# Optimization experiments

Measured on AMD Instinct MI355X. Metric: run time of the kernel, lower is better.

The kernel has to match this reference:

```python
import jax, jax.numpy as jnp
import numpy as np

D_MODEL = 1024
NUM_HEADS = 16
HEAD_DIM = D_MODEL // NUM_HEADS
THETA = 10000.0


def _init_linear(key, d_out, d_in):
    sigma = np.sqrt(2.0 / (d_in + d_out))
    w = jax.random.truncated_normal(key, -3.0, 3.0, (d_out, d_in), dtype=jnp.float32)
    return w * sigma


def setup_inputs() -> dict:
    key = jax.random.key(0)
    kh, kq, kk, kv, ko = jax.random.split(key, 5)
    h = jax.random.normal(kh, (2, 2048, D_MODEL), dtype=jnp.float32)
    return {
        "h": h,
        "wq": _init_linear(kq, D_MODEL, D_MODEL),
        "wk": _init_linear(kk, D_MODEL, D_MODEL),
        "wv": _init_linear(kv, D_MODEL, D_MODEL),
        "wo": _init_linear(ko, D_MODEL, D_MODEL),
    }


def _rope(x, pos):
    # x: [B, H, T, dh]; rotate interleaved pairs (..., 2k, 2k+1)
    dh = x.shape[-1]
    freq = THETA ** (-jnp.arange(0, dh // 2, dtype=jnp.float32) / (dh // 2))
    ang = pos[:, None] * freq[None, :]            # [T, dh/2]
    cos, sin = jnp.cos(ang), jnp.sin(ang)
    xr = x.reshape(*x.shape[:-1], dh // 2, 2)
    x0, x1 = xr[..., 0], xr[..., 1]
    out = jnp.stack((cos * x0 - sin * x1, sin * x0 + cos * x1), axis=-1)
    return out.reshape(x.shape)


def reference(h, wq, wk, wv, wo):
    B, T, D = h.shape
    Hn, dh = NUM_HEADS, HEAD_DIM

    def split_heads(x):  # [B,T,D] -> [B,H,T,dh]
        return x.reshape(B, T, Hn, dh).transpose(0, 2, 1, 3)

    Q = split_heads(h @ wq.T)
    K = split_heads(h @ wk.T)
    V = split_heads(h @ wv.T)

    pos = jnp.arange(T, dtype=jnp.float32)
    Q = _rope(Q, pos)
    K = _rope(K, pos)

    scores = jnp.einsum('bhqd,bhkd->bhqk', Q, K) / jnp.sqrt(jnp.float32(dh))
    mask = jnp.tril(jnp.ones((T, T), dtype=bool))
    scores = jnp.where(mask, scores, -jnp.inf)
    attn = jax.nn.softmax(scores, axis=-1)
    out = jnp.einsum('bhqk,bhkd->bhqd', attn, V)   # [B,H,T,dh]
    out = out.transpose(0, 2, 1, 3).reshape(B, T, D)
    return out @ wo.T
```

## Files before the change

kernel.cpp:

```cpp
#include <hip/hip_runtime.h>
#include <math.h>

typedef __bf16 bf16_t;
typedef __bf16 v8bf __attribute__((ext_vector_type(8)));
typedef __bf16 v4bf __attribute__((ext_vector_type(4)));
typedef float  v4f  __attribute__((ext_vector_type(4)));

#define AS1 __attribute__((address_space(1)))
#define AS3 __attribute__((address_space(3)))

static __device__ __forceinline__ void load_lds16(const bf16_t* g, bf16_t* l) {
    __builtin_amdgcn_global_load_lds((AS1 void*)const_cast<bf16_t*>(g),
                                     (AS3 void*)l, 16, 0, 0);
}
static __device__ __forceinline__ void load_lds16b(const char* g, char* l) {
    __builtin_amdgcn_global_load_lds((AS1 void*)const_cast<char*>(g),
                                     (AS3 void*)l, 16, 0, 0);
}

static __device__ __forceinline__ void fast_sincos(float ang, float* sn, float* cs) {
    float rv = ang * 0.15915494309189535f;
    rv -= floorf(rv);
    const float a = rv * 6.283185307179586f;
    *sn = __sinf(a);
    *cs = __cosf(a);
}

__global__ __launch_bounds__(256) void cvt_fp32_bf16(
    const float* __restrict__ h,  const float* __restrict__ wq,
    const float* __restrict__ wk, const float* __restrict__ wv,
    const float* __restrict__ wo,
    bf16_t* __restrict__ hb,  bf16_t* __restrict__ wqb,
    bf16_t* __restrict__ wkb, bf16_t* __restrict__ wvb,
    bf16_t* __restrict__ wob)
{
    const size_t HM = (size_t)4 << 20;
    const size_t i8 = ((size_t)blockIdx.x * 256 + threadIdx.x) * 8;
    const float* src; bf16_t* dst; size_t off;
    if (i8 < HM) { src = h; dst = hb; off = i8; }
    else {
        const size_t r = (i8 - HM) >> 20;
        off = (i8 - HM) & (((size_t)1 << 20) - 1);
        src = (r == 0) ? wq  : (r == 1) ? wk  : (r == 2) ? wv  : wo;
        dst = (r == 0) ? wqb : (r == 1) ? wkb : (r == 2) ? wvb : wob;
    }
    const float4 a = *(const float4*)(src + off);
    const float4 b = *(const float4*)(src + off + 4);
    v8bf o;
    o[0]=(bf16_t)a.x; o[1]=(bf16_t)a.y; o[2]=(bf16_t)a.z; o[3]=(bf16_t)a.w;
    o[4]=(bf16_t)b.x; o[5]=(bf16_t)b.y; o[6]=(bf16_t)b.z; o[7]=(bf16_t)b.w;
    *(v8bf*)(dst + off) = o;
}

__global__ __launch_bounds__(256) void qkv_gemm_rope(
    const bf16_t* __restrict__ A,
    const bf16_t* __restrict__ wq,
    const bf16_t* __restrict__ wk,
    const bf16_t* __restrict__ wv,
    bf16_t* __restrict__ qo, bf16_t* __restrict__ ko, bf16_t* __restrict__ vo)
{
    __shared__ __align__(16) bf16_t smem[17408];

    const int tid = threadIdx.x;
    const int n0  = blockIdx.x * 128;
    const int m0  = blockIdx.y * 128;
    const int sel = n0 >> 10;
    const bf16_t* W = (sel == 0) ? wq : (sel == 1) ? wk : wv;
    const int wr0 = n0 & 1023;

    const int wave = tid >> 6;
    const int lane = tid & 63;
    const int l16  = lane & 15;
    const int quad = lane >> 4;
    const int wrow = (wave >> 1) * 64;
    const int wcol = (wave & 1) * 64;

    v4f acc[4][4];
    #pragma unroll
    for (int i = 0; i < 4; ++i)
        #pragma unroll
        for (int j = 0; j < 4; ++j) acc[i][j] = (v4f)(0.0f);

    const int c0r  = tid >> 2;
    const int c0c  = (tid & 3) * 8;
    #define QKV_STAGE(bbuf, ktile)                                             \
        {                                                                      \
            const int k0_ = (ktile) * 32;                                      \
            load_lds16(A + (size_t)(m0 + c0r) * 1024 + k0_ + c0c,              \
                       smem + (bbuf) * 4096 + tid * 8);                        \
            load_lds16(A + (size_t)(m0 + 64 + c0r) * 1024 + k0_ + c0c,         \
                       smem + (bbuf) * 4096 + 2048 + tid * 8);                 \
            load_lds16(W + (size_t)(wr0 + c0r) * 1024 + k0_ + c0c,             \
                       smem + 8192 + (bbuf) * 4096 + tid * 8);                 \
            load_lds16(W + (size_t)(wr0 + 64 + c0r) * 1024 + k0_ + c0c,        \
                       smem + 8192 + (bbuf) * 4096 + 2048 + tid * 8);          \
        }

    QKV_STAGE(0, 0);
    for (int kt = 0; kt < 32; ++kt) {
        const int cur = kt & 1;
        __syncthreads();
        if (kt < 31) QKV_STAGE(cur ^ 1, kt + 1);

        const bf16_t* As = smem + cur * 4096;
        const bf16_t* Bs = smem + 8192 + cur * 4096;
        v8bf af[4], bfb[4];
        #pragma unroll
        for (int i = 0; i < 4; ++i) {
            af[i]  = *(const v8bf*)&As[(wrow + i * 16 + l16) * 32 + quad * 8];
            bfb[i] = *(const v8bf*)&Bs[(wcol + i * 16 + l16) * 32 + quad * 8];
        }
        #pragma unroll
        for (int i = 0; i < 4; ++i)
            #pragma unroll
            for (int j = 0; j < 4; ++j)
                acc[i][j] = __builtin_amdgcn_mfma_f32_16x16x32_bf16(
                    af[i], bfb[j], acc[i][j], 0, 0, 0);
    }
    __syncthreads();
    #undef QKV_STAGE

    bf16_t* Ls = smem + wave * 4352;
    const int bq     = (m0 + wrow) >> 11;
    const int hd     = ((n0 + wcol) >> 6) & 15;
    const int t_base = (m0 + wrow) & 2047;

    if (sel < 2) {
        bf16_t* OUT = (sel == 0) ? qo : ko;
        #pragma unroll
        for (int j = 0; j < 4; ++j) {
            const int dcol = j * 16 + l16;
            const int kk   = dcol >> 1;
            const float f  = exp2f((float)kk * -0.4152410118609203f);
            float cb, sb, c1, s1, c16, s16;
            fast_sincos((float)(t_base + quad * 4) * f, &sb, &cb);
            fast_sincos(f, &s1, &c1);
            fast_sincos(16.0f * f, &s16, &c16);
            float ci = cb, si = sb;
            #pragma unroll
            for (int i = 0; i < 4; ++i) {
                float cr = ci, sr = si;
                #pragma unroll
                for (int r = 0; r < 4; ++r) {
                    const int mrow = i * 16 + quad * 4 + r;
                    float v = acc[i][j][r];
                    const float vp = __shfl_xor(v, 1);
                    v = ((dcol & 1) == 0) ? (cr * v - sr * vp)
                                          : (sr * vp + cr * v);
                    Ls[mrow * 68 + dcol] = (bf16_t)v;
                    if (r < 3) {
                        const float cn = cr * c1 - sr * s1;
                        sr = sr * c1 + cr * s1;
                        cr = cn;
                    }
                }
                if (i < 3) {
                    const float cn = ci * c16 - si * s16;
                    si = si * c16 + ci * s16;
                    ci = cn;
                }
            }
        }
        #pragma unroll
        for (int s = 0; s < 8; ++s) {
            const int row = s * 8 + (lane >> 3);
            const int off = (lane & 7) * 8;
            const v8bf vv = *(const v8bf*)&Ls[row * 68 + off];
            *(v8bf*)(OUT + (((size_t)(bq * 16 + hd) * 2048) + t_base + row) * 64 + off) = vv;
        }
    } else {
        #pragma unroll
        for (int i = 0; i < 4; ++i)
            #pragma unroll
            for (int j = 0; j < 4; ++j) {
                v4bf p;
                #pragma unroll
                for (int r = 0; r < 4; ++r) p[r] = (bf16_t)acc[i][j][r];
                *(v4bf*)&Ls[(j * 16 + l16) * 68 + i * 16 + quad * 4] = p;
            }
        #pragma unroll
        for (int s = 0; s < 8; ++s) {
            const int drow = s * 8 + (lane >> 3);
            const int off  = (lane & 7) * 8;
            const v8bf vv = *(const v8bf*)&Ls[drow * 68 + off];
            *(v8bf*)(vo + (((size_t)(bq * 16 + hd) * 64) + drow) * 2048 + t_base + off) = vv;
        }
    }
}

__global__ __launch_bounds__(256, 4) void attn_mfma(
    const bf16_t* __restrict__ qg,
    const bf16_t* __restrict__ kg,
    const bf16_t* __restrict__ vtg,
    bf16_t* __restrict__ og)
{
    __shared__ __align__(16) bf16_t Ks[2][4096];
    __shared__ __align__(16) bf16_t Vs[2][4096];
    __shared__ __align__(16) bf16_t Ps[4][1024];

    const int tid  = threadIdx.x;
    const int wave = tid >> 6;
    const int lane = tid & 63;
    const int l16  = lane & 15;
    const int quad = lane >> 4;

    const int i   = blockIdx.x;
    const int xcd = i & 7;
    const int j   = i >> 3;
    const int bhl = j >> 5;
    const int u   = j & 31;
    const int q64 = (bhl & 1) ? (31 - u) : u;
    const int bh  = xcd * 4 + bhl;
    const int b = bh >> 4, hh = bh & 15;

    const char* Kb = (const char*)(kg  + (size_t)bh * 2048 * 64);
    const char* Vb = (const char*)(vtg + (size_t)bh * 64 * 2048);

    const int qglb = q64 * 64 + wave * 16 + l16;

    const int sw  = (l16 & 7) << 4;
    const int cb0 = (quad << 4) ^ sw;

    const int grow = tid >> 3;
    const int gsw  = ((tid & 7) << 4) ^ ((grow & 7) << 4);

    const bf16_t* qrow = qg + ((size_t)bh * 2048 + qglb) * 64;
    v8bf qf[2];
    qf[0] = *(const v8bf*)(qrow + quad * 8);
    qf[1] = *(const v8bf*)(qrow + 32 + quad * 8);
    #pragma unroll
    for (int e = 0; e < 8; ++e) {
        qf[0][e] = (bf16_t)((float)qf[0][e] * 0.18033688011112042f);
        qf[1][e] = (bf16_t)((float)qf[1][e] * 0.18033688011112042f);
    }

    v8bf ones1;
    #pragma unroll
    for (int e = 0; e < 8; ++e) ones1[e] = (bf16_t)1.0f;

    float m_r = -1e30f;
    v4f l_acc = (v4f)(0.0f);
    v4f o_acc[4];
    #pragma unroll
    for (int d = 0; d < 4; ++d) o_acc[d] = (v4f)(0.0f);

    {
        const char* ks = Kb + ((size_t)grow << 7) + gsw;
        const char* vs = Vb + ((size_t)grow << 12) + gsw;
        char* kd = (char*)Ks[0] + tid * 16;
        char* vd = (char*)Vs[0] + tid * 16;
        load_lds16b(ks, kd);
        load_lds16b(ks + (32 << 7), kd + 4096);
        load_lds16b(vs, vd);
        load_lds16b(vs + ((size_t)32 << 12), vd + 4096);
    }

    for (int kt = 0; kt <= q64; ++kt) {
        const int cur = kt & 1;
        const int nxt = cur ^ 1;
        __syncthreads();

        if (kt < q64) {
            const char* ks = Kb + ((size_t)((kt + 1) * 64 + grow) << 7) + gsw;
            const char* vs = Vb + ((size_t)grow << 12) + ((size_t)(kt + 1) << 7) + gsw;
            char* kd = (char*)Ks[nxt] + tid * 16;
            char* vd = (char*)Vs[nxt] + tid * 16;
            load_lds16b(ks, kd);
            load_lds16b(ks + (32 << 7), kd + 4096);
            load_lds16b(vs, vd);
            load_lds16b(vs + ((size_t)32 << 12), vd + 4096);
        }

        const char* ksc = (const char*)Ks[cur];
        v4f s_acc[4];
        #pragma unroll
        for (int kblk = 0; kblk < 4; ++kblk) s_acc[kblk] = (v4f)(0.0f);
        #pragma unroll
        for (int kblk = 0; kblk < 4; ++kblk) {
            const char* kr = ksc + ((kblk * 16 + l16) << 7);
            const v8bf kf0 = *(const v8bf*)(kr + cb0);
            const v8bf kf1 = *(const v8bf*)(kr + (cb0 ^ 64));
            s_acc[kblk] = __builtin_amdgcn_mfma_f32_16x16x32_bf16(
                kf0, qf[0], s_acc[kblk], 0, 0, 0);
            s_acc[kblk] = __builtin_amdgcn_mfma_f32_16x16x32_bf16(
                kf1, qf[1], s_acc[kblk], 0, 0, 0);
        }

        if (kt == q64) {
            #pragma unroll
            for (int kblk = 0; kblk < 4; ++kblk)
                #pragma unroll
                for (int r = 0; r < 4; ++r)
                    if (kt * 64 + kblk * 16 + quad * 4 + r > qglb)
                        s_acc[kblk][r] = -1e30f;
        }

        float mx = -1e30f;
        #pragma unroll
        for (int kblk = 0; kblk < 4; ++kblk)
            #pragma unroll
            for (int r = 0; r < 4; ++r) mx = fmaxf(mx, s_acc[kblk][r]);
        mx = fmaxf(mx, __shfl_xor(mx, 16));
        mx = fmaxf(mx, __shfl_xor(mx, 32));
        if (!__all(mx - m_r <= 8.0f)) {
            const float mn = fmaxf(m_r, mx);
            const float a  = exp2f(m_r - mn);
            m_r = mn;
            l_acc *= a;
            #pragma unroll
            for (int d = 0; d < 4; ++d) o_acc[d] *= a;
        }

        char* psc = (char*)Ps[wave] + (l16 << 7);
        #pragma unroll
        for (int kblk = 0; kblk < 4; ++kblk) {
            v4bf p;
            #pragma unroll
            for (int r = 0; r < 4; ++r)
                p[r] = (bf16_t)exp2f(s_acc[kblk][r] - m_r);
            *(v4bf*)(psc + ((kblk * 32 + quad * 8) ^ sw)) = p;
        }
        const v8bf pf0 = *(const v8bf*)(psc + cb0);
        const v8bf pf1 = *(const v8bf*)(psc + (cb0 ^ 64));

        const char* vsc = (const char*)Vs[cur];
        #pragma unroll
        for (int dblk = 0; dblk < 4; ++dblk) {
            const char* vr = vsc + ((dblk * 16 + l16) << 7);
            const v8bf vf0 = *(const v8bf*)(vr + cb0);
            const v8bf vf1 = *(const v8bf*)(vr + (cb0 ^ 64));
            o_acc[dblk] = __builtin_amdgcn_mfma_f32_16x16x32_bf16(
                vf0, pf0, o_acc[dblk], 0, 0, 0);
            o_acc[dblk] = __builtin_amdgcn_mfma_f32_16x16x32_bf16(
                vf1, pf1, o_acc[dblk], 0, 0, 0);
        }
        l_acc = __builtin_amdgcn_mfma_f32_16x16x32_bf16(ones1, pf0, l_acc, 0, 0, 0);
        l_acc = __builtin_amdgcn_mfma_f32_16x16x32_bf16(ones1, pf1, l_acc, 0, 0, 0);
    }

    const float inv_l = 1.0f / l_acc[0];
    const size_t base = ((size_t)b * 2048 + qglb) * 1024 + hh * 64;
    #pragma unroll
    for (int dblk = 0; dblk < 4; ++dblk) {
        v4bf o;
        #pragma unroll
        for (int r = 0; r < 4; ++r) o[r] = (bf16_t)(o_acc[dblk][r] * inv_l);
        *(v4bf*)(og + base + dblk * 16 + quad * 4) = o;
    }
}

__global__ __launch_bounds__(256) void out_gemm(
    const bf16_t* __restrict__ A,
    const bf16_t* __restrict__ W,
    float* __restrict__ C)
{
    __shared__ __align__(16) float smemf[6144];
    bf16_t* Sb = (bf16_t*)smemf;

    const int tid = threadIdx.x;
    const int n0  = blockIdx.x * 64;
    const int m0  = blockIdx.y * 128;

    const int wave = tid >> 6;
    const int lane = tid & 63;
    const int l16  = lane & 15;
    const int quad = lane >> 4;
    const int wrow = (wave >> 1) * 64;
    const int wcol = (wave & 1) * 32;

    v4f acc[4][2];
    #pragma unroll
    for (int i = 0; i < 4; ++i)
        #pragma unroll
        for (int j = 0; j < 2; ++j) acc[i][j] = (v4f)(0.0f);

    const int c0r = tid >> 2;
    const int c0c = (tid & 3) * 8;
    #define OUT_STAGE(bbuf, ktile)                                             \
        {                                                                      \
            const int k0_ = (ktile) * 32;                                      \
            load_lds16(A + (size_t)(m0 + c0r) * 1024 + k0_ + c0c,              \
                       Sb + (bbuf) * 4096 + tid * 8);                          \
            load_lds16(A + (size_t)(m0 + 64 + c0r) * 1024 + k0_ + c0c,         \
                       Sb + (bbuf) * 4096 + 2048 + tid * 8);                   \
            load_lds16(W + (size_t)(n0 + (tid >> 2)) * 1024 + k0_ + c0c,       \
                       Sb + 8192 + (bbuf) * 2048 + tid * 8);                   \
        }

    OUT_STAGE(0, 0);
    for (int kt = 0; kt < 32; ++kt) {
        const int cur = kt & 1;
        __syncthreads();
        if (kt < 31) OUT_STAGE(cur ^ 1, kt + 1);

        const bf16_t* As = Sb + cur * 4096;
        const bf16_t* Bs = Sb + 8192 + cur * 2048;
        v8bf af[4], bfb[2];
        #pragma unroll
        for (int i = 0; i < 4; ++i)
            af[i]  = *(const v8bf*)&As[(wrow + i * 16 + l16) * 32 + quad * 8];
        #pragma unroll
        for (int j = 0; j < 2; ++j)
            bfb[j] = *(const v8bf*)&Bs[(wcol + j * 16 + l16) * 32 + quad * 8];
        #pragma unroll
        for (int i = 0; i < 4; ++i)
            #pragma unroll
            for (int j = 0; j < 2; ++j)
                acc[i][j] = __builtin_amdgcn_mfma_f32_16x16x32_bf16(
                    af[i], bfb[j], acc[i][j], 0, 0, 0);
    }
    __syncthreads();
    #undef OUT_STAGE

    float* Lw = smemf + wave * 1088;
    #pragma unroll
    for (int half = 0; half < 2; ++half) {
        #pragma unroll
        for (int ii = 0; ii < 2; ++ii) {
            const int i = half * 2 + ii;
            #pragma unroll
            for (int j = 0; j < 2; ++j)
                #pragma unroll
                for (int r = 0; r < 4; ++r)
                    Lw[(ii * 16 + quad * 4 + r) * 34 + j * 16 + l16] = acc[i][j][r];
        }
        #pragma unroll
        for (int s = 0; s < 8; ++s) {
            const int row = s * 4 + (lane >> 4);
            const float2 vv = *(const float2*)&Lw[row * 34 + l16 * 2];
            *(float2*)(C + (size_t)(m0 + wrow + half * 32 + row) * 1024
                         + n0 + wcol + l16 * 2) = vv;
        }
    }
}

extern "C" void kernel_launch(void* const* d_in, const int* in_sizes, int n_in,
                              void* d_out, int out_size, void* d_ws, size_t ws_size,
                              hipStream_t stream) {
    const float* h  = (const float*)d_in[0];
    const float* wq = (const float*)d_in[1];
    const float* wk = (const float*)d_in[2];
    const float* wv = (const float*)d_in[3];
    const float* wo = (const float*)d_in[4];

    const size_t NH = (size_t)4096 * 1024;
    const size_t NW = (size_t)1024 * 1024;

    bf16_t* hb  = (bf16_t*)d_ws;
    bf16_t* wqb = hb  + NH;
    bf16_t* wkb = wqb + NW;
    bf16_t* wvb = wkb + NW;
    bf16_t* wob = wvb + NW;
    bf16_t* qw  = wob + NW;
    bf16_t* kw  = qw + NH;
    bf16_t* vw  = kw + NH;
    bf16_t* og  = hb;

    cvt_fp32_bf16<<<dim3(4096), dim3(256), 0, stream>>>(
        h, wq, wk, wv, wo, hb, wqb, wkb, wvb, wob);
    qkv_gemm_rope<<<dim3(24, 32), dim3(256), 0, stream>>>(
        hb, wqb, wkb, wvb, qw, kw, vw);
    attn_mfma<<<dim3(1024), dim3(256), 0, stream>>>(qw, kw, vw, og);
    out_gemm<<<dim3(16, 32), dim3(256), 0, stream>>>(og, wob, (float*)d_out);
}
```

Measured before the change: 186.6 us.

## Use single-buffered 128-key tiles in causal attention kernel

The attention kernel now processes 128 keys per iteration instead of 64. It drops the double-buffered K/V prefetch in favour of a single load-then-sync per tile, and launch bounds move from 4 to 3 waves per SIMD. This halves loop iterations and barriers and gives each wave more MFMA work per sync. In exchange, global-to-LDS loads no longer overlap compute, and for odd query tiles the last key tile computes a masked half that is thrown away.

```diff
diff --git a/kernel.cpp b/kernel.cpp
--- a/kernel.cpp
+++ b/kernel.cpp
@@ -188,15 +188,15 @@
     }
 }
 
-__global__ __launch_bounds__(256, 4) void attn_mfma(
+__global__ __launch_bounds__(256, 3) void attn_mfma(
     const bf16_t* __restrict__ qg,
     const bf16_t* __restrict__ kg,
     const bf16_t* __restrict__ vtg,
     bf16_t* __restrict__ og)
 {
-    __shared__ __align__(16) bf16_t Ks[2][4096];
-    __shared__ __align__(16) bf16_t Vs[2][4096];
-    __shared__ __align__(16) bf16_t Ps[4][1024];
+    __shared__ __align__(16) bf16_t Ks[8192];
+    __shared__ __align__(16) bf16_t Vs[8192];
+    __shared__ __align__(16) bf16_t Ps[4][2048];
 
     const int tid  = threadIdx.x;
     const int wave = tid >> 6;
@@ -209,20 +209,23 @@
     const int j   = i >> 3;
     const int bhl = j >> 5;
     const int u   = j & 31;
-    const int q64 = (bhl & 1) ? (31 - u) : u;
+    const int qt  = (bhl & 1) ? (31 - u) : u;
     const int bh  = xcd * 4 + bhl;
     const int b = bh >> 4, hh = bh & 15;
 
     const char* Kb = (const char*)(kg  + (size_t)bh * 2048 * 64);
     const char* Vb = (const char*)(vtg + (size_t)bh * 64 * 2048);
 
-    const int qglb = q64 * 64 + wave * 16 + l16;
+    const int qglb = qt * 64 + wave * 16 + l16;
+    const int ktb  = qt >> 1;
 
     const int sw  = (l16 & 7) << 4;
     const int cb0 = (quad << 4) ^ sw;
 
-    const int grow = tid >> 3;
-    const int gsw  = ((tid & 7) << 4) ^ ((grow & 7) << 4);
+    const int krow = tid >> 3;
+    const int kswb = ((tid & 7) << 4) ^ ((krow & 7) << 4);
+    const int vrow = tid >> 4;
+    const int vswb = ((tid & 15) << 4) ^ ((vrow & 7) << 4);
 
     const bf16_t* qrow = qg + ((size_t)bh * 2048 + qglb) * 64;
     v8bf qf[2];
@@ -244,40 +247,28 @@
     #pragma unroll
     for (int d = 0; d < 4; ++d) o_acc[d] = (v4f)(0.0f);
 
-    {
-        const char* ks = Kb + ((size_t)grow << 7) + gsw;
-        const char* vs = Vb + ((size_t)grow << 12) + gsw;
-        char* kd = (char*)Ks[0] + tid * 16;
-        char* vd = (char*)Vs[0] + tid * 16;
-        load_lds16b(ks, kd);
-        load_lds16b(ks + (32 << 7), kd + 4096);
-        load_lds16b(vs, vd);
-        load_lds16b(vs + ((size_t)32 << 12), vd + 4096);
-    }
-
-    for (int kt = 0; kt <= q64; ++kt) {
-        const int cur = kt & 1;
-        const int nxt = cur ^ 1;
+    for (int kt = 0; kt <= ktb; ++kt) {
+        if (kt) __syncthreads();
+
+        {
+            const char* ksrc = Kb + ((size_t)(kt * 128 + krow) << 7) + kswb;
+            const char* vsrc = Vb + ((size_t)vrow << 12) + ((size_t)kt << 8) + vswb;
+            char* kd = (char*)Ks + tid * 16;
+            char* vd = (char*)Vs + tid * 16;
+            #pragma unroll
+            for (int s = 0; s < 4; ++s) {
+                load_lds16b(ksrc + (size_t)s * (32 << 7), kd + s * 4096);
+                load_lds16b(vsrc + ((size_t)s << 16), vd + s * 4096);
+            }
+        }
         __syncthreads();
 
-        if (kt < q64) {
-            const char* ks = Kb + ((size_t)((kt + 1) * 64 + grow) << 7) + gsw;
-            const char* vs = Vb + ((size_t)grow << 12) + ((size_t)(kt + 1) << 7) + gsw;
-            char* kd = (char*)Ks[nxt] + tid * 16;
-            char* vd = (char*)Vs[nxt] + tid * 16;
-            load_lds16b(ks, kd);
-            load_lds16b(ks + (32 << 7), kd + 4096);
-            load_lds16b(vs, vd);
-            load_lds16b(vs + ((size_t)32 << 12), vd + 4096);
-        }
-
-        const char* ksc = (const char*)Ks[cur];
-        v4f s_acc[4];
-        #pragma unroll
-        for (int kblk = 0; kblk < 4; ++kblk) s_acc[kblk] = (v4f)(0.0f);
-        #pragma unroll
-        for (int kblk = 0; kblk < 4; ++kblk) {
-            const char* kr = ksc + ((kblk * 16 + l16) << 7);
+        v4f s_acc[8];
+        #pragma unroll
+        for (int kblk = 0; kblk < 8; ++kblk) s_acc[kblk] = (v4f)(0.0f);
+        #pragma unroll
+        for (int kblk = 0; kblk < 8; ++kblk) {
+            const char* kr = (const char*)Ks + ((kblk * 16 + l16) << 7);
             const v8bf kf0 = *(const v8bf*)(kr + cb0);
             const v8bf kf1 = *(const v8bf*)(kr + (cb0 ^ 64));
             s_acc[kblk] = __builtin_amdgcn_mfma_f32_16x16x32_bf16(
@@ -286,18 +277,18 @@
                 kf1, qf[1], s_acc[kblk], 0, 0, 0);
         }
 
-        if (kt == q64) {
-            #pragma unroll
-            for (int kblk = 0; kblk < 4; ++kblk)
+        if (kt == ktb) {
+            #pragma unroll
+            for (int kblk = 0; kblk < 8; ++kblk)
                 #pragma unroll
                 for (int r = 0; r < 4; ++r)
-                    if (kt * 64 + kblk * 16 + quad * 4 + r > qglb)
+                    if (kt * 128 + kblk * 16 + quad * 4 + r > qglb)
                         s_acc[kblk][r] = -1e30f;
         }
 
         float mx = -1e30f;
         #pragma unroll
-        for (int kblk = 0; kblk < 4; ++kblk)
+        for (int kblk = 0; kblk < 8; ++kblk)
             #pragma unroll
             for (int r = 0; r < 4; ++r) mx = fmaxf(mx, s_acc[kblk][r]);
         mx = fmaxf(mx, __shfl_xor(mx, 16));
@@ -311,31 +302,34 @@
             for (int d = 0; d < 4; ++d) o_acc[d] *= a;
         }
 
-        char* psc = (char*)Ps[wave] + (l16 << 7);
-        #pragma unroll
-        for (int kblk = 0; kblk < 4; ++kblk) {
+        char* psc = (char*)Ps[wave] + (l16 << 8);
+        #pragma unroll
+        for (int kblk = 0; kblk < 8; ++kblk) {
             v4bf p;
             #pragma unroll
             for (int r = 0; r < 4; ++r)
                 p[r] = (bf16_t)exp2f(s_acc[kblk][r] - m_r);
-            *(v4bf*)(psc + ((kblk * 32 + quad * 8) ^ sw)) = p;
-        }
-        const v8bf pf0 = *(const v8bf*)(psc + cb0);
-        const v8bf pf1 = *(const v8bf*)(psc + (cb0 ^ 64));
-
-        const char* vsc = (const char*)Vs[cur];
+            *(v4bf*)(psc + (((kblk << 5) + (quad << 3)) ^ sw)) = p;
+        }
+        v8bf pf[4];
+        #pragma unroll
+        for (int ks = 0; ks < 4; ++ks)
+            pf[ks] = *(const v8bf*)(psc + (((ks << 6) + (quad << 4)) ^ sw));
+
         #pragma unroll
         for (int dblk = 0; dblk < 4; ++dblk) {
-            const char* vr = vsc + ((dblk * 16 + l16) << 7);
-            const v8bf vf0 = *(const v8bf*)(vr + cb0);
-            const v8bf vf1 = *(const v8bf*)(vr + (cb0 ^ 64));
-            o_acc[dblk] = __builtin_amdgcn_mfma_f32_16x16x32_bf16(
-                vf0, pf0, o_acc[dblk], 0, 0, 0);
-            o_acc[dblk] = __builtin_amdgcn_mfma_f32_16x16x32_bf16(
-                vf1, pf1, o_acc[dblk], 0, 0, 0);
-        }
-        l_acc = __builtin_amdgcn_mfma_f32_16x16x32_bf16(ones1, pf0, l_acc, 0, 0, 0);
-        l_acc = __builtin_amdgcn_mfma_f32_16x16x32_bf16(ones1, pf1, l_acc, 0, 0, 0);
+            const char* vr = (const char*)Vs + ((dblk * 16 + l16) << 8);
+            #pragma unroll
+            for (int ks = 0; ks < 4; ++ks) {
+                const v8bf vf = *(const v8bf*)(vr + (((ks << 6) + (quad << 4)) ^ sw));
+                o_acc[dblk] = __builtin_amdgcn_mfma_f32_16x16x32_bf16(
+                    vf, pf[ks], o_acc[dblk], 0, 0, 0);
+            }
+        }
+        #pragma unroll
+        for (int ks = 0; ks < 4; ++ks)
+            l_acc = __builtin_amdgcn_mfma_f32_16x16x32_bf16(
+                ones1, pf[ks], l_acc, 0, 0, 0);
     }
 
     const float inv_l = 1.0f / l_acc[0];
```

New measurement: 194.1 us. 1.04x slower.

## Split attention KV tile across wave pairs with 32-row Q per wave and merge

Applied to the files above, without the earlier changes.

Restructures the attention kernel so each pair of waves shares 32 query rows, with each wave handling half of every 64-key tile, and merges the partial softmax states through LDS at the end. Each K/V fragment loaded from LDS now feeds two MFMAs (two query chunks), which halves LDS reads per MFMA. On the diagonal tile, the wave whose keys all lie beyond its queries skips that tile. The cost is more accumulator registers per wave, a final cross-wave reduction with two extra barriers, and some imbalance between the two halves on the diagonal tile.

```diff
diff --git a/kernel.cpp b/kernel.cpp
--- a/kernel.cpp
+++ b/kernel.cpp
@@ -196,13 +196,15 @@
 {
     __shared__ __align__(16) bf16_t Ks[2][4096];
     __shared__ __align__(16) bf16_t Vs[2][4096];
-    __shared__ __align__(16) bf16_t Ps[4][1024];
+    __shared__ __align__(16) bf16_t Ps[8][512];
 
     const int tid  = threadIdx.x;
     const int wave = tid >> 6;
     const int lane = tid & 63;
     const int l16  = lane & 15;
     const int quad = lane >> 4;
+    const int pr   = wave >> 1;
+    const int hf   = wave & 1;
 
     const int i   = blockIdx.x;
     const int xcd = i & 7;
@@ -216,33 +218,41 @@
     const char* Kb = (const char*)(kg  + (size_t)bh * 2048 * 64);
     const char* Vb = (const char*)(vtg + (size_t)bh * 64 * 2048);
 
-    const int qglb = q64 * 64 + wave * 16 + l16;
+    const int q0 = q64 * 64 + pr * 32;
 
     const int sw  = (l16 & 7) << 4;
+    const int sw4 = (l16 & 3) << 4;
     const int cb0 = (quad << 4) ^ sw;
+    const int vb0 = ((hf << 6) | (quad << 4)) ^ sw;
 
     const int grow = tid >> 3;
     const int gsw  = ((tid & 7) << 4) ^ ((grow & 7) << 4);
 
-    const bf16_t* qrow = qg + ((size_t)bh * 2048 + qglb) * 64;
-    v8bf qf[2];
-    qf[0] = *(const v8bf*)(qrow + quad * 8);
-    qf[1] = *(const v8bf*)(qrow + 32 + quad * 8);
+    v8bf qf[2][2];
     #pragma unroll
-    for (int e = 0; e < 8; ++e) {
-        qf[0][e] = (bf16_t)((float)qf[0][e] * 0.18033688011112042f);
-        qf[1][e] = (bf16_t)((float)qf[1][e] * 0.18033688011112042f);
+    for (int qc = 0; qc < 2; ++qc) {
+        const bf16_t* qrow = qg + ((size_t)bh * 2048 + q0 + qc * 16 + l16) * 64;
+        qf[qc][0] = *(const v8bf*)(qrow + quad * 8);
+        qf[qc][1] = *(const v8bf*)(qrow + 32 + quad * 8);
+        #pragma unroll
+        for (int e = 0; e < 8; ++e) {
+            qf[qc][0][e] = (bf16_t)((float)qf[qc][0][e] * 0.18033688011112042f);
+            qf[qc][1][e] = (bf16_t)((float)qf[qc][1][e] * 0.18033688011112042f);
+        }
     }
 
     v8bf ones1;
     #pragma unroll
     for (int e = 0; e < 8; ++e) ones1[e] = (bf16_t)1.0f;
 
-    float m_r = -1e30f;
-    v4f l_acc = (v4f)(0.0f);
-    v4f o_acc[4];
+    float m_r[2] = {-1e30f, -1e30f};
+    v4f l_acc[2];
+    l_acc[0] = (v4f)(0.0f); l_acc[1] = (v4f)(0.0f);
+    v4f o_acc[2][4];
     #pragma unroll
-    for (int d = 0; d < 4; ++d) o_acc[d] = (v4f)(0.0f);
+    for (int qc = 0; qc < 2; ++qc)
+        #pragma unroll
+        for (int d = 0; d < 4; ++d) o_acc[qc][d] = (v4f)(0.0f);
 
     {
         const char* ks = Kb + ((size_t)grow << 7) + gsw;
@@ -271,81 +281,123 @@
             load_lds16b(vs + ((size_t)32 << 12), vd + 4096);
         }
 
-        const char* ksc = (const char*)Ks[cur];
-        v4f s_acc[4];
-        #pragma unroll
-        for (int kblk = 0; kblk < 4; ++kblk) s_acc[kblk] = (v4f)(0.0f);
-        #pragma unroll
-        for (int kblk = 0; kblk < 4; ++kblk) {
-            const char* kr = ksc + ((kblk * 16 + l16) << 7);
-            const v8bf kf0 = *(const v8bf*)(kr + cb0);
-            const v8bf kf1 = *(const v8bf*)(kr + (cb0 ^ 64));
-            s_acc[kblk] = __builtin_amdgcn_mfma_f32_16x16x32_bf16(
-                kf0, qf[0], s_acc[kblk], 0, 0, 0);
-            s_acc[kblk] = __builtin_amdgcn_mfma_f32_16x16x32_bf16(
-                kf1, qf[1], s_acc[kblk], 0, 0, 0);
-        }
-
-        if (kt == q64) {
-            #pragma unroll
-            for (int kblk = 0; kblk < 4; ++kblk)
+        const bool active = !(pr == 0 && hf == 1 && kt == q64);
+        if (active) {
+            const char* ksc = (const char*)Ks[cur];
+            v4f s_acc[2][2];
+            s_acc[0][0] = (v4f)(0.0f); s_acc[0][1] = (v4f)(0.0f);
+            s_acc[1][0] = (v4f)(0.0f); s_acc[1][1] = (v4f)(0.0f);
+            #pragma unroll
+            for (int kb2 = 0; kb2 < 2; ++kb2) {
+                const char* kr = ksc + (((hf * 2 + kb2) * 16 + l16) << 7);
+                const v8bf kf0 = *(const v8bf*)(kr + cb0);
+                const v8bf kf1 = *(const v8bf*)(kr + (cb0 ^ 64));
+                s_acc[0][kb2] = __builtin_amdgcn_mfma_f32_16x16x32_bf16(
+                    kf0, qf[0][0], s_acc[0][kb2], 0, 0, 0);
+                s_acc[1][kb2] = __builtin_amdgcn_mfma_f32_16x16x32_bf16(
+                    kf0, qf[1][0], s_acc[1][kb2], 0, 0, 0);
+                s_acc[0][kb2] = __builtin_amdgcn_mfma_f32_16x16x32_bf16(
+                    kf1, qf[0][1], s_acc[0][kb2], 0, 0, 0);
+                s_acc[1][kb2] = __builtin_amdgcn_mfma_f32_16x16x32_bf16(
+                    kf1, qf[1][1], s_acc[1][kb2], 0, 0, 0);
+            }
+
+            if (kt == q64) {
+                #pragma unroll
+                for (int qc = 0; qc < 2; ++qc)
+                    #pragma unroll
+                    for (int kb2 = 0; kb2 < 2; ++kb2)
+                        #pragma unroll
+                        for (int r = 0; r < 4; ++r)
+                            if (kt * 64 + (hf * 2 + kb2) * 16 + quad * 4 + r >
+                                q0 + qc * 16 + l16)
+                                s_acc[qc][kb2][r] = -1e30f;
+            }
+
+            v8bf pf[2];
+            #pragma unroll
+            for (int qc = 0; qc < 2; ++qc) {
+                float mx = fmaxf(
+                    fmaxf(fmaxf(s_acc[qc][0][0], s_acc[qc][0][1]),
+                          fmaxf(s_acc[qc][0][2], s_acc[qc][0][3])),
+                    fmaxf(fmaxf(s_acc[qc][1][0], s_acc[qc][1][1]),
+                          fmaxf(s_acc[qc][1][2], s_acc[qc][1][3])));
+                mx = fmaxf(mx, __shfl_xor(mx, 16));
+                mx = fmaxf(mx, __shfl_xor(mx, 32));
+                if (!__all(mx - m_r[qc] <= 8.0f)) {
+                    const float mn = fmaxf(m_r[qc], mx);
+                    const float a  = exp2f(m_r[qc] - mn);
+                    m_r[qc] = mn;
+                    l_acc[qc] *= a;
+                    #pragma unroll
+                    for (int d = 0; d < 4; ++d) o_acc[qc][d] *= a;
+                }
+                char* psc = (char*)Ps[wave * 2 + qc] + (l16 << 6);
+                #pragma unroll
+                for (int kb2 = 0; kb2 < 2; ++kb2) {
+                    v4bf p;
+                    #pragma unroll
+                    for (int r = 0; r < 4; ++r)
+                        p[r] = (bf16_t)exp2f(s_acc[qc][kb2][r] - m_r[qc]);
+                    *(v4bf*)(psc + ((kb2 * 32 + quad * 8) ^ sw4)) = p;
+                }
+                pf[qc] = *(const v8bf*)(psc + ((quad << 4) ^ sw4));
+            }
+
+            const char* vsc = (const char*)Vs[cur];
+            #pragma unroll
+            for (int dblk = 0; dblk < 4; ++dblk) {
+                const char* vr = vsc + ((dblk * 16 + l16) << 7);
+                const v8bf vf = *(const v8bf*)(vr + vb0);
+                o_acc[0][dblk] = __builtin_amdgcn_mfma_f32_16x16x32_bf16(
+                    vf, pf[0], o_acc[0][dblk], 0, 0, 0);
+                o_acc[1][dblk] = __builtin_amdgcn_mfma_f32_16x16x32_bf16(
+                    vf, pf[1], o_acc[1][dblk], 0, 0, 0);
+            }
+            l_acc[0] = __builtin_amdgcn_mfma_f32_16x16x32_bf16(
+                ones1, pf[0], l_acc[0], 0, 0, 0);
+            l_acc[1] = __builtin_amdgcn_mfma_f32_16x16x32_bf16(
+                ones1, pf[1], l_acc[1], 0, 0, 0);
+        }
+    }
+
+    __syncthreads();
+    float* OF = (float*)Ks;
+    float* MF = (float*)Vs;
+    if (hf == 1) {
+        float* o = OF + (pr * 64 + lane) * 32;
+        #pragma unroll
+        for (int qc = 0; qc < 2; ++qc)
+            #pragma unroll
+            for (int d = 0; d < 4; ++d)
+                *(v4f*)(o + qc * 16 + d * 4) = o_acc[qc][d];
+        float* ml = MF + (pr * 64 + lane) * 4;
+        ml[0] = m_r[0]; ml[1] = l_acc[0][0];
+        ml[2] = m_r[1]; ml[3] = l_acc[1][0];
+    }
+    __syncthreads();
+    if (hf == 0) {
+        const float* o  = OF + (pr * 64 + lane) * 32;
+        const float* ml = MF + (pr * 64 + lane) * 4;
+        #pragma unroll
+        for (int qc = 0; qc < 2; ++qc) {
+            const float m1 = ml[qc * 2], l1 = ml[qc * 2 + 1];
+            const float ms = fmaxf(m_r[qc], m1);
+            const float a0 = exp2f(m_r[qc] - ms);
+            const float a1 = exp2f(m1 - ms);
+            const float li = 1.0f / (l_acc[qc][0] * a0 + l1 * a1);
+            const size_t base =
+                ((size_t)b * 2048 + q0 + qc * 16 + l16) * 1024 + hh * 64;
+            #pragma unroll
+            for (int d = 0; d < 4; ++d) {
+                const v4f o1 = *(const v4f*)(o + qc * 16 + d * 4);
+                v4bf ob;
                 #pragma unroll
                 for (int r = 0; r < 4; ++r)
-                    if (kt * 64 + kblk * 16 + quad * 4 + r > qglb)
-                        s_acc[kblk][r] = -1e30f;
-        }
-
-        float mx = -1e30f;
-        #pragma unroll
-        for (int kblk = 0; kblk < 4; ++kblk)
-            #pragma unroll
-            for (int r = 0; r < 4; ++r) mx = fmaxf(mx, s_acc[kblk][r]);
-        mx = fmaxf(mx, __shfl_xor(mx, 16));
-        mx = fmaxf(mx, __shfl_xor(mx, 32));
-        if (!__all(mx - m_r <= 8.0f)) {
-            const float mn = fmaxf(m_r, mx);
-            const float a  = exp2f(m_r - mn);
-            m_r = mn;
-            l_acc *= a;
-            #pragma unroll
-            for (int d = 0; d < 4; ++d) o_acc[d] *= a;
-        }
-
-        char* psc = (char*)Ps[wave] + (l16 << 7);
-        #pragma unroll
-        for (int kblk = 0; kblk < 4; ++kblk) {
-            v4bf p;
-            #pragma unroll
-            for (int r = 0; r < 4; ++r)
-                p[r] = (bf16_t)exp2f(s_acc[kblk][r] - m_r);
-            *(v4bf*)(psc + ((kblk * 32 + quad * 8) ^ sw)) = p;
-        }
-        const v8bf pf0 = *(const v8bf*)(psc + cb0);
-        const v8bf pf1 = *(const v8bf*)(psc + (cb0 ^ 64));
-
-        const char* vsc = (const char*)Vs[cur];
-        #pragma unroll
-        for (int dblk = 0; dblk < 4; ++dblk) {
-            const char* vr = vsc + ((dblk * 16 + l16) << 7);
-            const v8bf vf0 = *(const v8bf*)(vr + cb0);
-            const v8bf vf1 = *(const v8bf*)(vr + (cb0 ^ 64));
-            o_acc[dblk] = __builtin_amdgcn_mfma_f32_16x16x32_bf16(
-                vf0, pf0, o_acc[dblk], 0, 0, 0);
-            o_acc[dblk] = __builtin_amdgcn_mfma_f32_16x16x32_bf16(
-                vf1, pf1, o_acc[dblk], 0, 0, 0);
-        }
-        l_acc = __builtin_amdgcn_mfma_f32_16x16x32_bf16(ones1, pf0, l_acc, 0, 0, 0);
-        l_acc = __builtin_amdgcn_mfma_f32_16x16x32_bf16(ones1, pf1, l_acc, 0, 0, 0);
-    }
-
-    const float inv_l = 1.0f / l_acc[0];
-    const size_t base = ((size_t)b * 2048 + qglb) * 1024 + hh * 64;
-    #pragma unroll
-    for (int dblk = 0; dblk < 4; ++dblk) {
-        v4bf o;
-        #pragma unroll
-        for (int r = 0; r < 4; ++r) o[r] = (bf16_t)(o_acc[dblk][r] * inv_l);
-        *(v4bf*)(og + base + dblk * 16 + quad * 4) = o;
+                    ob[r] = (bf16_t)((o_acc[qc][d][r] * a0 + o1[r] * a1) * li);
+                *(v4bf*)(og + base + d * 16 + quad * 4) = ob;
+            }
+        }
     }
 }
 
```

Result: slower. 190.6 us (+2.1%).
